# Performance work log

Measured on AMD Instinct MI355X. Metric: run time of the kernel, lower is better.

Reference implementation:

```python
import jax, jax.numpy as jnp
import numpy as np

RATE = 22050.0 / 256.0  # audio_target_rate from the torch source
SIZES = [2.23147392 * RATE, 2.62519274 * RATE, 3.74199546 * RATE,
         5.78800454 * RATE, 8.02371882 * RATE, float('inf')]
WEIGHT = 1.0
EPS = 1e-7


def _giou_1d(a, b):
    # a, b: [P, 2] intervals (start, end); elementwise 1-D GIoU
    inter = jnp.clip(jnp.minimum(a[:, 1], b[:, 1]) - jnp.maximum(a[:, 0], b[:, 0]), 0.0)
    union = (a[:, 1] - a[:, 0]) + (b[:, 1] - b[:, 0]) - inter
    iou = inter / (union + EPS)
    enclose = jnp.maximum(a[:, 1], b[:, 1]) - jnp.minimum(a[:, 0], b[:, 0])
    return iou - (enclose - union) / (enclose + EPS)


def setup_inputs() -> dict:
    key = jax.random.key(0)
    ks = jax.random.split(key, 4)
    B, N = 4, 32
    L0 = 131072  # frames at the finest level
    levels = 6
    anchors = {f"anchors_l{i}": (jnp.arange(L0 >> i, dtype=jnp.float32) + 0.5) * (2.0 ** i)
               for i in range(levels)}
    A = sum(int(v.shape[0]) for v in anchors.values())  # 258048
    # GT intervals: all rows belong to class 0 (matches class_id filter in the source)
    starts = jax.random.uniform(ks[0], (B, N), minval=0.0, maxval=float(L0) - 2000.0)
    lens = jax.random.uniform(ks[1], (B, N), minval=50.0, maxval=1500.0)
    annotations = jnp.stack([starts, starts + lens, jnp.zeros((B, N))], axis=-1).astype(jnp.float32)
    # Predicted intervals for every anchor
    c = jax.random.uniform(ks[2], (B, A), minval=0.0, maxval=float(L0))
    w = jax.random.uniform(ks[3], (B, A), minval=10.0, maxval=2000.0)
    regressions = jnp.stack([c - 0.5 * w, c + 0.5 * w], axis=-1).astype(jnp.float32)
    out = {"regressions": regressions, "annotations": annotations, "class_id": 0}
    out.update(anchors)
    return out


def reference(regressions, annotations, anchors_l0, anchors_l1, anchors_l2,
              anchors_l3, anchors_l4, anchors_l5, class_id):
    anchors_list = [anchors_l0, anchors_l1, anchors_l2, anchors_l3, anchors_l4, anchors_l5]
    all_pts = jnp.concatenate(anchors_list)  # [A]

    def per_sample(reg, ann):
        # ann: [N, 3]; inputs guarantee every row has class == class_id and is valid
        order = jnp.argsort(ann[:, 1] - ann[:, 0])  # sort GT by length ascending
        ann = ann[order]
        s, e = ann[:, 0:1], ann[:, 1:2]  # [N,1]
        pos_parts, nl_parts, nr_parts = [], [], []
        for i, pts in enumerate(anchors_list):
            l = pts[None, :] - s            # [N, A_i]
            r = e - pts[None, :]            # [N, A_i]
            in_gt = (l >= 0.0) & (r >= 0.0)
            m = jnp.maximum(l, r)
            lower = SIZES[i - 1] if i > 0 else 0.0
            cand = in_gt & (m >= lower) & (m < SIZES[i])
            pos_parts.append(cand.any(axis=0))
            amax = jnp.argmax(cand, axis=0)  # first True per anchor (0 if none)
            inv = 1.0 / (2.0 ** i)           # normalize l*/r* by 2**level
            nl_parts.append(jnp.take_along_axis(l, amax[None, :], axis=0)[0] * inv)
            nr_parts.append(jnp.take_along_axis(r, amax[None, :], axis=0)[0] * inv)
        pos = jnp.concatenate(pos_parts)   # [A] bool
        nl = jnp.concatenate(nl_parts)     # [A]
        nr = jnp.concatenate(nr_parts)     # [A]
        # decoded normalized target boxes around the anchor points
        boxes = jnp.stack([all_pts - nl, all_pts + nr], axis=1)  # [A, 2]
        giou = jnp.clip(_giou_1d(boxes, reg[:, :2]), -1.0, 1.0)
        loss = 1.0 - giou
        posf = pos.astype(loss.dtype)
        # masked mean over positive anchors (torch indexes by boolean mask then .mean())
        return jnp.sum(loss * posf) / jnp.maximum(jnp.sum(posf), 1.0) * WEIGHT

    return jax.vmap(per_sample)(regressions, annotations)  # [B] per-sample losses
```

## Files before the change

kernel.cpp:

```cpp
#include <hip/hip_runtime.h>

#define EPS_F 1e-7f
#define NN 32
#define MARGIN 3
#define NSEG (NN * 6)
#define TPB 1024
#define CAND_MAX 24576

__global__ __launch_bounds__(TPB) void rl_fused(
    const float* __restrict__ reg,
    const float* __restrict__ ann,
    int c0, int A,
    float* __restrict__ out)
{
    const int b = blockIdx.x;
    const int t = threadIdx.x;
    const int wave = t >> 6;
    const int lane = t & 63;

    __shared__ float2 sh_se[NN];
    __shared__ int4   seg[NSEG];
    __shared__ int    pfx[NSEG];
    __shared__ unsigned segmask[NSEG];
    __shared__ unsigned cand32[CAND_MAX / 4];
    __shared__ float  sh_sz[8];
    __shared__ float  red_l[TPB / 64], red_p[TPB / 64];

    if (t < 8) {
        const float szc[8] = {
            0.0f,
            (float)(2.23147392 * (22050.0 / 256.0)),
            (float)(2.62519274 * (22050.0 / 256.0)),
            (float)(3.74199546 * (22050.0 / 256.0)),
            (float)(5.78800454 * (22050.0 / 256.0)),
            (float)(8.02371882 * (22050.0 / 256.0)),
            __builtin_inff(), __builtin_inff()
        };
        sh_sz[t] = szc[t];
    }

    if (t < NN) {
        const float* an = ann + (size_t)b * (size_t)NN * 3;
        const float s0 = an[t * 3 + 0];
        const float e0 = an[t * 3 + 1];
        const float len = e0 - s0;
        int rank = 0;
#pragma unroll
        for (int j = 0; j < NN; ++j) {
            const float lj = __shfl(len, j, 64);
            rank += (lj < len) || (lj == len && j < t);
        }
        sh_se[rank] = make_float2(s0, e0);
    }
    __syncthreads();

    if (t < NSEG) {
        const int n   = t / 6;
        const int lvl = t - n * 6;
        const float2 se = sh_se[n];
        const float s = se.x, e = se.y;
        const float mid   = 0.5f * (s + e);
        const float halfL = 0.5f * (e - s);
        const float lo = sh_sz[lvl];
        const float hi = sh_sz[lvl + 1];
        const int   cnt = c0 >> lvl;
        const float inv   = __int_as_float((127 - lvl) << 23);
        const float scale = __int_as_float((127 + lvl) << 23);

        const float dlo = fmaxf(lo - halfL, 0.0f);
        const float dhi = hi - halfL;
        const float prl = fmaxf(mid + dlo, s);
        const float prh = fminf(mid + dhi, e);
        const float pll = fmaxf(mid - dhi, s);
        const float plh = fminf(mid - dlo, e);

        int r0 = (int)floorf(prl * inv - 0.5f) - MARGIN;
        int r1 = (int)floorf(prh * inv - 0.5f) + MARGIN;
        int l0 = (int)floorf(pll * inv - 0.5f) - MARGIN;
        int l1 = (int)floorf(plh * inv - 0.5f) + MARGIN;
        r0 = max(r0, 0); r1 = min(r1, cnt - 1);
        l0 = max(l0, 0); l1 = min(l1, cnt - 1);
        if (r1 >= r0) l1 = min(l1, r0 - 1);
        const int lenL = max(l1 - l0 + 1, 0);
        const int lenR = max(r1 - r0 + 1, 0);
        seg[t] = make_int4(l0, r0, lenL | (lenR << 16), (n << 8) | lvl);
        pfx[t] = lenL + lenR;

        const int firstloc = lenL ? l0 : r0;
        const int lastloc  = lenR ? r1 : l1;
        const float ptmin = ((float)firstloc + 0.5f) * scale;
        const float ptmax = ((float)lastloc  + 0.5f) * scale;
        unsigned msk = 0u;
        for (int n2 = 0; n2 < n; ++n2) {
            const float2 o = sh_se[n2];
            if ((o.x <= ptmax) & (o.y >= ptmin)) msk |= (1u << n2);
        }
        segmask[t] = msk;
    }
    __syncthreads();

    if (wave == 0) {
        int carry = 0;
#pragma unroll
        for (int k = 0; k < 3; ++k) {
            int v = pfx[k * 64 + lane];
#pragma unroll
            for (int o = 1; o < 64; o <<= 1) {
                const int u = __shfl_up(v, o, 64);
                v += (lane >= o) ? u : 0;
            }
            pfx[k * 64 + lane] = v + carry;
            carry += __shfl(v, 63, 64);
        }
    }
    __syncthreads();
    const int T = min(pfx[NSEG - 1], CAND_MAX);

    if (t < NSEG) {
        const int4 sg = seg[t];
        const int count = (sg.z & 0xffff) + (sg.z >> 16);
        const int start = pfx[t] - count;
        seg[t].w = sg.w | (start << 16);
        unsigned char* cb = (unsigned char*)cand32;
        int i = start;
        const int end = min(start + count, CAND_MAX);
        const unsigned rep = 0x01010101u * (unsigned)t;
        while (i < end && (i & 3)) cb[i++] = (unsigned char)t;
        for (; i + 4 <= end; i += 4) cand32[i >> 2] = rep;
        for (; i < end; ++i) cb[i] = (unsigned char)t;
    }
    __syncthreads();

    const int twoc0 = 2 * c0;
    const unsigned char* cb = (const unsigned char*)cand32;
    float loss_sum = 0.0f, pos_sum = 0.0f;

    for (int j = t; j < T; j += TPB) {
        const int sid = cb[j];
        const int4 sg = seg[sid];
        unsigned msk = segmask[sid];
        const int lenL  = sg.z & 0xffff;
        const int start = (int)(((unsigned)sg.w) >> 16);
        const int n     = (sg.w >> 8) & 0xff;
        const int lvl   = sg.w & 0xff;
        const int local = j - start;
        const int loc = (local < lenL) ? (sg.x + local) : (sg.y + (local - lenL));
        const float scale = __int_as_float((127 + lvl) << 23);
        const float inv   = __int_as_float((127 - lvl) << 23);
        const int aoff = twoc0 - (twoc0 >> lvl);

        const float2 g = ((const float2*)reg)[(size_t)b * A + (aoff + loc)];

        const float pt = ((float)loc + 0.5f) * scale;
        const float lo = sh_sz[lvl];
        const float hi = sh_sz[lvl + 1];
        const float2 se = sh_se[n];
        const float l = pt - se.x;
        const float r = se.y - pt;
        const float m = fmaxf(l, r);
        bool valid = (fminf(l, r) >= 0.0f) & (m >= lo) & (m < hi);

        while (valid && msk) {
            const int n2 = __builtin_ctz(msk);
            msk &= msk - 1u;
            const float2 o = sh_se[n2];
            const float l2 = pt - o.x;
            const float r2 = o.y - pt;
            const float m2 = fmaxf(l2, r2);
            if ((fminf(l2, r2) >= 0.0f) & (m2 >= lo) & (m2 < hi)) valid = false;
        }

        const float b0 = pt - l * inv;
        const float b1 = pt + r * inv;
        const float inter = fmaxf(fminf(b1, g.y) - fmaxf(b0, g.x), 0.0f);
        const float uni = (b1 - b0) + (g.y - g.x) - inter;
        const float iou = inter * __builtin_amdgcn_rcpf(uni + EPS_F);
        const float enc = fmaxf(b1, g.y) - fminf(b0, g.x);
        float giou = iou - (enc - uni) * __builtin_amdgcn_rcpf(enc + EPS_F);
        giou = fminf(fmaxf(giou, -1.0f), 1.0f);
        loss_sum += valid ? (1.0f - giou) : 0.0f;
        pos_sum  += valid ? 1.0f : 0.0f;
    }

    for (int o = 32; o > 0; o >>= 1) {
        loss_sum += __shfl_down(loss_sum, o, 64);
        pos_sum  += __shfl_down(pos_sum,  o, 64);
    }
    if (lane == 0) { red_l[wave] = loss_sum; red_p[wave] = pos_sum; }
    __syncthreads();
    if (t < 16) {
        float Ls = red_l[t];
        float Ps = red_p[t];
#pragma unroll
        for (int o = 8; o > 0; o >>= 1) {
            Ls += __shfl_down(Ls, o, 16);
            Ps += __shfl_down(Ps, o, 16);
        }
        if (t == 0) out[b] = Ls / fmaxf(Ps, 1.0f);
    }
}

extern "C" void kernel_launch(void* const* d_in, const int* in_sizes, int n_in,
                              void* d_out, int out_size, void* d_ws, size_t ws_size,
                              hipStream_t stream) {
    const float* reg = (const float*)d_in[0];
    const float* ann = (const float*)d_in[1];
    const int c0 = in_sizes[3];
    const int A = in_sizes[3] + in_sizes[4] + in_sizes[5] +
                  in_sizes[6] + in_sizes[7] + in_sizes[8];
    const int B = out_size;
    (void)d_ws; (void)ws_size;

    rl_fused<<<dim3(B), TPB, 0, stream>>>(reg, ann, c0, A, (float*)d_out);
}
```

Before: 76.48 us.

## Split per-sample candidate loop across cooperative blocks with grid-sync reduction

Replaces the one-block-per-sample launch (1024 threads) with a cooperative grid of 8 slices × B blocks of 256 threads. Each block redundantly rebuilds the GT sort, segment table and candidate map, then handles a strided slice of the candidate anchors. Per-block partial sums go to workspace, and after a grid-wide sync slice 0 combines them. The aim is to spread the main gather/GIoU loop over more CUs, at the cost of duplicated setup, workspace atomics and cooperative launch and sync overhead.

```diff
diff --git a/kernel.cpp b/kernel.cpp
--- a/kernel.cpp
+++ b/kernel.cpp
@@ -1,19 +1,26 @@
 #include <hip/hip_runtime.h>
+#include <hip/hip_cooperative_groups.h>
+
+namespace cg = cooperative_groups;
 
 #define EPS_F 1e-7f
 #define NN 32
 #define MARGIN 3
 #define NSEG (NN * 6)
-#define TPB 1024
+#define TPB 256
+#define SLICES 8
 #define CAND_MAX 24576
 
-__global__ __launch_bounds__(TPB) void rl_fused(
+__global__ __launch_bounds__(TPB) void rl_coop(
     const float* __restrict__ reg,
     const float* __restrict__ ann,
     int c0, int A,
+    float* __restrict__ ws,
     float* __restrict__ out)
 {
-    const int b = blockIdx.x;
+    const int s_blk = blockIdx.x;
+    const int gridS = gridDim.x;
+    const int b = blockIdx.y;
     const int t = threadIdx.x;
     const int wave = t >> 6;
     const int lane = t & 63;
@@ -121,13 +128,13 @@
         const int count = (sg.z & 0xffff) + (sg.z >> 16);
         const int start = pfx[t] - count;
         seg[t].w = sg.w | (start << 16);
-        unsigned char* cb = (unsigned char*)cand32;
+        unsigned char* cbw = (unsigned char*)cand32;
         int i = start;
         const int end = min(start + count, CAND_MAX);
         const unsigned rep = 0x01010101u * (unsigned)t;
-        while (i < end && (i & 3)) cb[i++] = (unsigned char)t;
+        while (i < end && (i & 3)) cbw[i++] = (unsigned char)t;
         for (; i + 4 <= end; i += 4) cand32[i >> 2] = rep;
-        for (; i < end; ++i) cb[i] = (unsigned char)t;
+        for (; i < end; ++i) cbw[i] = (unsigned char)t;
     }
     __syncthreads();
 
@@ -135,7 +142,7 @@
     const unsigned char* cb = (const unsigned char*)cand32;
     float loss_sum = 0.0f, pos_sum = 0.0f;
 
-    for (int j = t; j < T; j += TPB) {
+    for (int j = s_blk * TPB + t; j < T; j += gridS * TPB) {
         const int sid = cb[j];
         const int4 sg = seg[sid];
         unsigned msk = segmask[sid];
@@ -188,15 +195,35 @@
     }
     if (lane == 0) { red_l[wave] = loss_sum; red_p[wave] = pos_sum; }
     __syncthreads();
-    if (t < 16) {
-        float Ls = red_l[t];
-        float Ps = red_p[t];
-#pragma unroll
-        for (int o = 8; o > 0; o >>= 1) {
-            Ls += __shfl_down(Ls, o, 16);
-            Ps += __shfl_down(Ps, o, 16);
-        }
-        if (t == 0) out[b] = Ls / fmaxf(Ps, 1.0f);
+
+    if (gridS == 1) {
+        if (t == 0) {
+            float Ls = 0.0f, Ps = 0.0f;
+#pragma unroll
+            for (int w = 0; w < TPB / 64; ++w) { Ls += red_l[w]; Ps += red_p[w]; }
+            out[b] = Ls / fmaxf(Ps, 1.0f);
+        }
+        return;
+    }
+
+    if (t == 0) {
+        float Ls = 0.0f, Ps = 0.0f;
+#pragma unroll
+        for (int w = 0; w < TPB / 64; ++w) { Ls += red_l[w]; Ps += red_p[w]; }
+        float* slot = ws + ((size_t)b * gridS + s_blk) * 2;
+        atomicExch(&slot[0], Ls);
+        atomicExch(&slot[1], Ps);
+    }
+    cg::this_grid().sync();
+
+    if (s_blk == 0 && t == 0) {
+        float Ls = 0.0f, Ps = 0.0f;
+        for (int i = 0; i < gridS; ++i) {
+            float* slot = ws + ((size_t)b * gridS + i) * 2;
+            Ls += atomicAdd(&slot[0], 0.0f);
+            Ps += atomicAdd(&slot[1], 0.0f);
+        }
+        out[b] = Ls / fmaxf(Ps, 1.0f);
     }
 }
 
@@ -209,7 +236,14 @@
     const int A = in_sizes[3] + in_sizes[4] + in_sizes[5] +
                   in_sizes[6] + in_sizes[7] + in_sizes[8];
     const int B = out_size;
-    (void)d_ws; (void)ws_size;
-
-    rl_fused<<<dim3(B), TPB, 0, stream>>>(reg, ann, c0, A, (float*)d_out);
+    float* ws = (float*)d_ws;
+    float* outp = (float*)d_out;
+
+    void* args[] = { (void*)&reg, (void*)&ann, (void*)&c0, (void*)&A,
+                     (void*)&ws, (void*)&outp };
+    hipError_t err = hipLaunchCooperativeKernel(
+        (const void*)rl_coop, dim3(SLICES, B), dim3(TPB), args, 0, stream);
+    if (err != hipSuccess) {
+        rl_coop<<<dim3(1, B), TPB, 0, stream>>>(reg, ann, c0, A, ws, outp);
+    }
 }
```

Measured after the change: 111.2 us. +45.5%, slower.
